# Kernel tuning notes

Measured on AMD Instinct MI355X. Metric: run time of the kernel, lower is better.

The kernel has to match this reference:

```python
import jax, jax.numpy as jnp
import numpy as np

B, IN, H = 4096, 1024, 1024


def setup_inputs() -> dict:
    key = jax.random.key(0)
    ks = jax.random.split(key, 16)
    s_in = 1.0 / np.sqrt(IN)
    s_h = 1.0 / np.sqrt(H)
    d = {
        "x_t": jax.random.normal(ks[0], (B, IN), jnp.float32),
        "h_prev": jax.random.normal(ks[1], (B, H), jnp.float32),
        "c_prev": jax.random.normal(ks[2], (B, H), jnp.float32),
    }
    # input->hidden weights (with bias), stored torch-style as (out, in)
    for i, name in enumerate(["ii", "if", "ig", "io"]):
        d[f"W_{name}"] = jax.random.uniform(ks[3 + i], (H, IN), jnp.float32, -s_in, s_in)
        d[f"b_{name}"] = jax.random.uniform(ks[7 + i], (H,), jnp.float32, -s_in, s_in)
    # hidden->hidden weights (no bias)
    for i, name in enumerate(["hi", "hf", "hg", "ho"]):
        d[f"W_{name}"] = jax.random.uniform(ks[11 + i], (H, H), jnp.float32, -s_h, s_h)
    return d


def reference(x_t, h_prev, c_prev,
              W_ii, b_ii, W_if, b_if, W_ig, b_ig, W_io, b_io,
              W_hi, W_hf, W_hg, W_ho):
    # Fuse the 8 small GEMMs into 2 concatenated GEMMs (same math).
    Wx = jnp.concatenate([W_ii, W_if, W_ig, W_io], axis=0)   # (4H, IN)
    Wh = jnp.concatenate([W_hi, W_hf, W_hg, W_ho], axis=0)   # (4H, H)
    b = jnp.concatenate([b_ii, b_if, b_ig, b_io], axis=0)    # (4H,)
    gates = x_t @ Wx.T + h_prev @ Wh.T + b                    # (B, 4H)
    zi, zf, zg, zo = jnp.split(gates, 4, axis=1)
    i_t = jax.nn.sigmoid(zi)
    f_t = jax.nn.sigmoid(zf)
    g_t = jnp.tanh(zg)
    o_t = jax.nn.sigmoid(zo)
    c_t = f_t * c_prev + i_t * g_t
    h_t = o_t * jnp.tanh(c_t)
    return (h_t, c_t, (i_t, f_t, g_t, o_t))
```

## Files before the change

### kernel.cpp

```cpp
#include <hip/hip_runtime.h>

#define B_DIM 4096
#define K_TOT 2048
#define H_DIM 1024

typedef short bf16x8 __attribute__((ext_vector_type(8)));
typedef float f32x4 __attribute__((ext_vector_type(4)));
typedef unsigned short u16x8 __attribute__((ext_vector_type(8)));

typedef __attribute__((address_space(1))) const unsigned gas_u32;
typedef __attribute__((address_space(3))) unsigned las_u32;

static __device__ __forceinline__ unsigned short f2bf(float f) {
  union { float f; unsigned u; } v; v.f = f;
  unsigned r = v.u + 0x7FFF + ((v.u >> 16) & 1);
  return (unsigned short)(r >> 16);
}

__global__ void pack_all(const float* __restrict__ x, const float* __restrict__ hp,
                         const float* __restrict__ W0, const float* __restrict__ W1,
                         const float* __restrict__ W2, const float* __restrict__ W3,
                         const float* __restrict__ W4, const float* __restrict__ W5,
                         const float* __restrict__ W6, const float* __restrict__ W7,
                         u16x8* __restrict__ A, u16x8* __restrict__ Wc) {
  const int t = blockIdx.x * blockDim.x + threadIdx.x;
  const int NA = (B_DIM * K_TOT) >> 3;
  const float* src;
  u16x8* dst;
  if (t < NA) {
    int idx = t << 3;
    int b = idx >> 11;
    int k = idx & 2047;
    src = (k < 1024) ? (x + b * 1024 + k) : (hp + b * 1024 + (k - 1024));
    dst = A + t;
  } else {
    int u = t - NA;
    int idx = u << 3;
    int n = idx >> 11;
    int k = idx & 2047;
    int gate = n >> 10;
    int j = n & 1023;
    int s = (k < 1024) ? gate : gate + 4;
    const float* base =
        (s == 0) ? W0 : (s == 1) ? W1 : (s == 2) ? W2 : (s == 3) ? W3 :
        (s == 4) ? W4 : (s == 5) ? W5 : (s == 6) ? W6 : W7;
    src = base + j * 1024 + (k & 1023);
    dst = Wc + u;
  }
  float4 lo = *(const float4*)src;
  float4 hi = *(const float4*)(src + 4);
  u16x8 v;
  v[0] = f2bf(lo.x); v[1] = f2bf(lo.y); v[2] = f2bf(lo.z); v[3] = f2bf(lo.w);
  v[4] = f2bf(hi.x); v[5] = f2bf(hi.y); v[6] = f2bf(hi.z); v[7] = f2bf(hi.w);
  *dst = v;
}

static __device__ __forceinline__ float sigm(float x) {
  return 1.0f / (1.0f + __expf(-x));
}
static __device__ __forceinline__ float tanh_fast(float x) {
  x = fminf(fmaxf(x, -15.f), 15.f);
  float t = __expf(-2.0f * x);
  return (1.0f - t) / (1.0f + t);
}

__global__ __launch_bounds__(256) void gemm_lstm(
    const unsigned short* __restrict__ A,
    const unsigned short* __restrict__ W,
    const float* __restrict__ cp,
    const float* __restrict__ bii, const float* __restrict__ bif,
    const float* __restrict__ big, const float* __restrict__ bio,
    float* __restrict__ out) {
  __shared__ unsigned short As[2][128 * 32];
  __shared__ unsigned short Bs[2][128 * 32];
  const int tid = threadIdx.x;
  const int wave = tid >> 6;
  const int lane = tid & 63;
  const int m0 = blockIdx.y << 7;
  const int j0 = blockIdx.x << 5;
  const int wm = (wave >> 1) << 6;
  const int wj16 = (wave & 1) << 4;

  f32x4 acc[4][4];
#pragma unroll
  for (int mi = 0; mi < 4; ++mi)
#pragma unroll
    for (int ni = 0; ni < 4; ++ni)
      acc[mi][ni] = (f32x4){0.f, 0.f, 0.f, 0.f};

  const int c0 = wave * 2;
  const int lr = lane >> 2;
  const int ls = lane & 3;
  const int g  = ls ^ ((lr >> 1) & 3);
  const unsigned short* aptr0 = A + (long)(m0 + c0 * 16 + lr) * K_TOT + g * 8;
  const unsigned short* aptr1 = aptr0 + 16 * K_TOT;
  const int rr0 = c0 * 16 + lr;
  const int rr1 = rr0 + 16;
  const unsigned short* bptr0 =
      W + (long)((rr0 >> 5) * 1024 + j0 + (rr0 & 31)) * K_TOT + g * 8;
  const unsigned short* bptr1 =
      W + (long)((rr1 >> 5) * 1024 + j0 + (rr1 & 31)) * K_TOT + g * 8;
  const int stg_off = c0 * 1024;

#define STAGE(buf, kk)                                                                   \
  do {                                                                                   \
    char* la = (char*)As + (buf) * 8192 + stg_off;                                       \
    char* lb = (char*)Bs + (buf) * 8192 + stg_off;                                       \
    __builtin_amdgcn_global_load_lds((gas_u32*)(aptr0 + (kk)), (las_u32*)la, 16, 0, 0);  \
    __builtin_amdgcn_global_load_lds((gas_u32*)(aptr1 + (kk)), (las_u32*)(la + 1024), 16, 0, 0); \
    __builtin_amdgcn_global_load_lds((gas_u32*)(bptr0 + (kk)), (las_u32*)lb, 16, 0, 0);  \
    __builtin_amdgcn_global_load_lds((gas_u32*)(bptr1 + (kk)), (las_u32*)(lb + 1024), 16, 0, 0); \
  } while (0)

  const int fr = lane & 15;
  const int gg = lane >> 4;
  const int sl = (gg ^ ((fr >> 1) & 3)) * 16;

  STAGE(0, 0);
  __syncthreads();

  int cur = 0;
  for (int k0 = 0; k0 < K_TOT; k0 += 32) {
    if (k0 + 32 < K_TOT) STAGE(cur ^ 1, k0 + 32);
    const char* baseA = (const char*)As + cur * 8192;
    const char* baseB = (const char*)Bs + cur * 8192;
    bf16x8 af[4], bfv[4];
#pragma unroll
    for (int i = 0; i < 4; ++i) {
      af[i]  = *(const bf16x8*)(baseA + (wm + i * 16 + fr) * 64 + sl);
      bfv[i] = *(const bf16x8*)(baseB + (i * 32 + wj16 + fr) * 64 + sl);
    }
#pragma unroll
    for (int mi = 0; mi < 4; ++mi)
#pragma unroll
      for (int ni = 0; ni < 4; ++ni)
        acc[mi][ni] = __builtin_amdgcn_mfma_f32_16x16x32_bf16(af[mi], bfv[ni], acc[mi][ni], 0, 0, 0);
    __syncthreads();
    cur ^= 1;
  }
#undef STAGE

  const int ccol = lane & 15;
  const int crow = (lane >> 4) * 4;
  const int j = j0 + wj16 + ccol;
  const float bi = bii[j];
  const float bff = bif[j];
  const float bg = big[j];
  const float bo = bio[j];
  const long BH = (long)B_DIM * H_DIM;
#pragma unroll
  for (int mi = 0; mi < 4; ++mi) {
#pragma unroll
    for (int reg = 0; reg < 4; ++reg) {
      const int row = m0 + wm + mi * 16 + crow + reg;
      const long p = (long)row * H_DIM + j;
      const float cvp = cp[p];
      const float iv = sigm(acc[mi][0][reg] + bi);
      const float fv = sigm(acc[mi][1][reg] + bff);
      const float gv = tanh_fast(acc[mi][2][reg] + bg);
      const float ov = sigm(acc[mi][3][reg] + bo);
      const float cv = fv * cvp + iv * gv;
      const float hv = ov * tanh_fast(cv);
      __builtin_nontemporal_store(hv, &out[p]);
      __builtin_nontemporal_store(cv, &out[BH + p]);
      __builtin_nontemporal_store(iv, &out[2 * BH + p]);
      __builtin_nontemporal_store(fv, &out[3 * BH + p]);
      __builtin_nontemporal_store(gv, &out[4 * BH + p]);
      __builtin_nontemporal_store(ov, &out[5 * BH + p]);
    }
  }
}

extern "C" void kernel_launch(void* const* d_in, const int* in_sizes, int n_in,
                              void* d_out, int out_size, void* d_ws, size_t ws_size,
                              hipStream_t stream) {
  const float* x    = (const float*)d_in[0];
  const float* h    = (const float*)d_in[1];
  const float* c    = (const float*)d_in[2];
  const float* W_ii = (const float*)d_in[3];
  const float* b_ii = (const float*)d_in[4];
  const float* W_if = (const float*)d_in[5];
  const float* b_if = (const float*)d_in[6];
  const float* W_ig = (const float*)d_in[7];
  const float* b_ig = (const float*)d_in[8];
  const float* W_io = (const float*)d_in[9];
  const float* b_io = (const float*)d_in[10];
  const float* W_hi = (const float*)d_in[11];
  const float* W_hf = (const float*)d_in[12];
  const float* W_hg = (const float*)d_in[13];
  const float* W_ho = (const float*)d_in[14];

  unsigned short* Abf = (unsigned short*)d_ws;
  unsigned short* Wbf = (unsigned short*)((char*)d_ws + (size_t)16 * 1024 * 1024);

  pack_all<<<8192, 256, 0, stream>>>(x, h, W_ii, W_if, W_ig, W_io,
                                     W_hi, W_hf, W_hg, W_ho,
                                     (u16x8*)Abf, (u16x8*)Wbf);
  dim3 grid(H_DIM / 32, B_DIM / 128);
  gemm_lstm<<<grid, 256, 0, stream>>>(Abf, Wbf, c, b_ii, b_if, b_ig, b_io,
                                      (float*)d_out);
}
```

Measured before the change: 287.6 us.

## Enlarge GEMM tile to 256x256 with deep multi-stage LDS pipeline

```diff
diff --git a/kernel.cpp b/kernel.cpp
--- a/kernel.cpp
+++ b/kernel.cpp
@@ -34,18 +34,21 @@
     src = (k < 1024) ? (x + b * 1024 + k) : (hp + b * 1024 + (k - 1024));
     dst = A + t;
   } else {
-    int u = t - NA;
-    int idx = u << 3;
-    int n = idx >> 11;
+    int u_ = t - NA;
+    int idx = u_ << 3;
+    int R = idx >> 11;
     int k = idx & 2047;
-    int gate = n >> 10;
-    int j = n & 1023;
+    int uu = R & 255;
+    int gate = (uu >> 4) & 3;
+    int ngg = uu >> 6;
+    int cc = uu & 15;
+    int j = (R >> 8) * 64 + ngg * 16 + cc;
     int s = (k < 1024) ? gate : gate + 4;
     const float* base =
         (s == 0) ? W0 : (s == 1) ? W1 : (s == 2) ? W2 : (s == 3) ? W3 :
         (s == 4) ? W4 : (s == 5) ? W5 : (s == 6) ? W6 : W7;
     src = base + j * 1024 + (k & 1023);
-    dst = Wc + u;
+    dst = Wc + u_;
   }
   float4 lo = *(const float4*)src;
   float4 hi = *(const float4*)(src + 4);
@@ -64,95 +67,142 @@
   return (1.0f - t) / (1.0f + t);
 }
 
-__global__ __launch_bounds__(256) void gemm_lstm(
+__global__ __launch_bounds__(512, 2) void gemm_lstm(
     const unsigned short* __restrict__ A,
     const unsigned short* __restrict__ W,
     const float* __restrict__ cp,
     const float* __restrict__ bii, const float* __restrict__ bif,
     const float* __restrict__ big, const float* __restrict__ bio,
     float* __restrict__ out) {
-  __shared__ unsigned short As[2][128 * 32];
-  __shared__ unsigned short Bs[2][128 * 32];
+  extern __shared__ char lds[];
   const int tid = threadIdx.x;
-  const int wave = tid >> 6;
+  const int w = tid >> 6;
   const int lane = tid & 63;
-  const int m0 = blockIdx.y << 7;
-  const int j0 = blockIdx.x << 5;
-  const int wm = (wave >> 1) << 6;
-  const int wj16 = (wave & 1) << 4;
-
-  f32x4 acc[4][4];
-#pragma unroll
-  for (int mi = 0; mi < 4; ++mi)
-#pragma unroll
-    for (int ni = 0; ni < 4; ++ni)
-      acc[mi][ni] = (f32x4){0.f, 0.f, 0.f, 0.f};
-
-  const int c0 = wave * 2;
-  const int lr = lane >> 2;
-  const int ls = lane & 3;
-  const int g  = ls ^ ((lr >> 1) & 3);
-  const unsigned short* aptr0 = A + (long)(m0 + c0 * 16 + lr) * K_TOT + g * 8;
-  const unsigned short* aptr1 = aptr0 + 16 * K_TOT;
-  const int rr0 = c0 * 16 + lr;
-  const int rr1 = rr0 + 16;
-  const unsigned short* bptr0 =
-      W + (long)((rr0 >> 5) * 1024 + j0 + (rr0 & 31)) * K_TOT + g * 8;
-  const unsigned short* bptr1 =
-      W + (long)((rr1 >> 5) * 1024 + j0 + (rr1 & 31)) * K_TOT + g * 8;
-  const int stg_off = c0 * 1024;
-
-#define STAGE(buf, kk)                                                                   \
-  do {                                                                                   \
-    char* la = (char*)As + (buf) * 8192 + stg_off;                                       \
-    char* lb = (char*)Bs + (buf) * 8192 + stg_off;                                       \
-    __builtin_amdgcn_global_load_lds((gas_u32*)(aptr0 + (kk)), (las_u32*)la, 16, 0, 0);  \
-    __builtin_amdgcn_global_load_lds((gas_u32*)(aptr1 + (kk)), (las_u32*)(la + 1024), 16, 0, 0); \
-    __builtin_amdgcn_global_load_lds((gas_u32*)(bptr0 + (kk)), (las_u32*)lb, 16, 0, 0);  \
-    __builtin_amdgcn_global_load_lds((gas_u32*)(bptr1 + (kk)), (las_u32*)(lb + 1024), 16, 0, 0); \
-  } while (0)
+  const int wm = w >> 2;
+  const int ng = w & 3;
+  const int bx = blockIdx.x;
+  const int by = blockIdx.y;
+
+  f32x4 acc[8][4];
+#pragma unroll
+  for (int i = 0; i < 8; ++i)
+#pragma unroll
+    for (int n = 0; n < 4; ++n)
+      acc[i][n] = (f32x4){0.f, 0.f, 0.f, 0.f};
+
+  const int v0 = tid, v1 = tid + 512;
+  const int r0 = v0 >> 2, g0 = (v0 & 3) ^ ((r0 >> 1) & 3);
+  const int r1 = v1 >> 2, g1 = (v1 & 3) ^ ((r1 >> 1) & 3);
+  const unsigned short* srcA0 = A + (long)(by * 256 + r0) * K_TOT + g0 * 8;
+  const unsigned short* srcA1 = A + (long)(by * 256 + r1) * K_TOT + g1 * 8;
+  const unsigned short* srcB0 = W + (long)(bx * 256 + r0) * K_TOT + g0 * 8;
+  const unsigned short* srcB1 = W + (long)(bx * 256 + r1) * K_TOT + g1 * 8;
+  const int d0 = v0 << 4, d1 = v1 << 4;
 
   const int fr = lane & 15;
   const int gg = lane >> 4;
-  const int sl = (gg ^ ((fr >> 1) & 3)) * 16;
-
-  STAGE(0, 0);
-  __syncthreads();
-
-  int cur = 0;
-  for (int k0 = 0; k0 < K_TOT; k0 += 32) {
-    if (k0 + 32 < K_TOT) STAGE(cur ^ 1, k0 + 32);
-    const char* baseA = (const char*)As + cur * 8192;
-    const char* baseB = (const char*)Bs + cur * 8192;
-    bf16x8 af[4], bfv[4];
-#pragma unroll
-    for (int i = 0; i < 4; ++i) {
-      af[i]  = *(const bf16x8*)(baseA + (wm + i * 16 + fr) * 64 + sl);
-      bfv[i] = *(const bf16x8*)(baseB + (i * 32 + wj16 + fr) * 64 + sl);
-    }
-#pragma unroll
-    for (int mi = 0; mi < 4; ++mi)
-#pragma unroll
-      for (int ni = 0; ni < 4; ++ni)
-        acc[mi][ni] = __builtin_amdgcn_mfma_f32_16x16x32_bf16(af[mi], bfv[ni], acc[mi][ni], 0, 0, 0);
-    __syncthreads();
-    cur ^= 1;
-  }
+  const int aoff = fr * 64 + ((gg ^ ((fr >> 1) & 3)) << 4);
+  const int wmoff = wm << 13;
+  const int ngoff = ng << 12;
+
+  bf16x8 bfr[4];
+
+#define STAGE(H)                                                               \
+  {                                                                            \
+    const int H_ = (H);                                                        \
+    const int koff_ = (H_ >> 1) * 32;                                          \
+    char* dst_ = lds + (((H_ >> 2) & 1) << 16) + ((H_ & 1) << 15) +            \
+                 (((H_ >> 1) & 1) << 14);                                      \
+    if (H_ & 1) {                                                              \
+      __builtin_amdgcn_global_load_lds((gas_u32*)(srcB0 + koff_),              \
+                                       (las_u32*)(dst_ + d0), 16, 0, 0);       \
+      __builtin_amdgcn_global_load_lds((gas_u32*)(srcB1 + koff_),              \
+                                       (las_u32*)(dst_ + d1), 16, 0, 0);       \
+    } else {                                                                   \
+      __builtin_amdgcn_global_load_lds((gas_u32*)(srcA0 + koff_),              \
+                                       (las_u32*)(dst_ + d0), 16, 0, 0);       \
+      __builtin_amdgcn_global_load_lds((gas_u32*)(srcA1 + koff_),              \
+                                       (las_u32*)(dst_ + d1), 16, 0, 0);       \
+    }                                                                          \
+  }
+
+#define G8 asm volatile("s_waitcnt vmcnt(8)" ::: "memory")
+#define G4 asm volatile("s_waitcnt vmcnt(4)" ::: "memory")
+#define G0 asm volatile("s_waitcnt vmcnt(0)" ::: "memory")
+#define GN ((void)0)
+
+#define DO_PHASE(P, KT, GUARD, DOSTAGE)                                        \
+  {                                                                            \
+    const char* lA_ = ldsbuf + ((P) >> 1) * 16384;                             \
+    const char* lB_ = ldsbuf + 32768 + ((P) >> 1) * 16384;                     \
+    bf16x8 af_[4];                                                             \
+    _Pragma("unroll")                                                          \
+    for (int i_ = 0; i_ < 4; ++i_)                                             \
+      af_[i_] = *(const bf16x8*)(lA_ + wmoff + (((P) & 1) * 4 + i_) * 1024 + aoff); \
+    if (((P) & 1) == 0) {                                                      \
+      _Pragma("unroll")                                                        \
+      for (int n_ = 0; n_ < 4; ++n_)                                           \
+        bfr[n_] = *(const bf16x8*)(lB_ + ngoff + n_ * 1024 + aoff);            \
+    }                                                                          \
+    if (DOSTAGE) STAGE((KT) * 4 + (P) + 6);                                    \
+    GUARD;                                                                     \
+    __builtin_amdgcn_s_barrier();                                              \
+    asm volatile("s_waitcnt lgkmcnt(0)" ::: "memory");                         \
+    __builtin_amdgcn_sched_barrier(0);                                         \
+    __builtin_amdgcn_s_setprio(1);                                             \
+    _Pragma("unroll")                                                          \
+    for (int i_ = 0; i_ < 4; ++i_) {                                           \
+      _Pragma("unroll")                                                        \
+      for (int n_ = 0; n_ < 4; ++n_)                                           \
+        acc[((P) & 1) * 4 + i_][n_] = __builtin_amdgcn_mfma_f32_16x16x32_bf16( \
+            af_[i_], bfr[n_], acc[((P) & 1) * 4 + i_][n_], 0, 0, 0);           \
+    }                                                                          \
+    __builtin_amdgcn_s_setprio(0);                                             \
+    __builtin_amdgcn_s_barrier();                                              \
+  }
+
+  STAGE(0); STAGE(1); STAGE(2); STAGE(3); STAGE(4); STAGE(5);
+  asm volatile("s_waitcnt vmcnt(8)" ::: "memory");
+  __builtin_amdgcn_s_barrier();
+
+  for (int kt = 0; kt < 30; ++kt) {
+    const char* ldsbuf = lds + ((kt & 1) << 16);
+    DO_PHASE(0, kt, GN, 1);
+    DO_PHASE(1, kt, G8, 1);
+    DO_PHASE(2, kt, GN, 1);
+    DO_PHASE(3, kt, G8, 1);
+  }
+  {
+    const char* ldsbuf = lds;
+    DO_PHASE(0, 30, GN, 1);
+    DO_PHASE(1, 30, G8, 1);
+    DO_PHASE(2, 30, GN, 0);
+    DO_PHASE(3, 30, G4, 0);
+  }
+  {
+    const char* ldsbuf = lds + 65536;
+    DO_PHASE(0, 31, GN, 0);
+    DO_PHASE(1, 31, G0, 0);
+    DO_PHASE(2, 31, GN, 0);
+    DO_PHASE(3, 31, GN, 0);
+  }
+#undef DO_PHASE
 #undef STAGE
 
   const int ccol = lane & 15;
-  const int crow = (lane >> 4) * 4;
-  const int j = j0 + wj16 + ccol;
+  const int crow = (lane >> 4) << 2;
+  const int j = (bx << 6) + (ng << 4) + ccol;
   const float bi = bii[j];
   const float bff = bif[j];
   const float bg = big[j];
   const float bo = bio[j];
   const long BH = (long)B_DIM * H_DIM;
-#pragma unroll
-  for (int mi = 0; mi < 4; ++mi) {
+  const int row0 = (by << 8) + (wm << 7) + crow;
+#pragma unroll
+  for (int mi = 0; mi < 8; ++mi) {
 #pragma unroll
     for (int reg = 0; reg < 4; ++reg) {
-      const int row = m0 + wm + mi * 16 + crow + reg;
+      const int row = row0 + mi * 16 + reg;
       const long p = (long)row * H_DIM + j;
       const float cvp = cp[p];
       const float iv = sigm(acc[mi][0][reg] + bi);
@@ -161,12 +211,12 @@
       const float ov = sigm(acc[mi][3][reg] + bo);
       const float cv = fv * cvp + iv * gv;
       const float hv = ov * tanh_fast(cv);
-      __builtin_nontemporal_store(hv, &out[p]);
-      __builtin_nontemporal_store(cv, &out[BH + p]);
-      __builtin_nontemporal_store(iv, &out[2 * BH + p]);
-      __builtin_nontemporal_store(fv, &out[3 * BH + p]);
-      __builtin_nontemporal_store(gv, &out[4 * BH + p]);
-      __builtin_nontemporal_store(ov, &out[5 * BH + p]);
+      out[p]          = hv;
+      out[BH + p]     = cv;
+      out[2 * BH + p] = iv;
+      out[3 * BH + p] = fv;
+      out[4 * BH + p] = gv;
+      out[5 * BH + p] = ov;
     }
   }
 }
@@ -193,10 +243,17 @@
   unsigned short* Abf = (unsigned short*)d_ws;
   unsigned short* Wbf = (unsigned short*)((char*)d_ws + (size_t)16 * 1024 * 1024);
 
+  static bool s_attr = false;
+  if (!s_attr) {
+    hipFuncSetAttribute((const void*)gemm_lstm,
+                        hipFuncAttributeMaxDynamicSharedMemorySize, 131072);
+    s_attr = true;
+  }
+
   pack_all<<<8192, 256, 0, stream>>>(x, h, W_ii, W_if, W_ig, W_io,
                                      W_hi, W_hf, W_hg, W_ho,
                                      (u16x8*)Abf, (u16x8*)Wbf);
-  dim3 grid(H_DIM / 32, B_DIM / 128);
-  gemm_lstm<<<grid, 256, 0, stream>>>(Abf, Wbf, c, b_ii, b_if, b_ig, b_io,
-                                      (float*)d_out);
-}
+  dim3 grid(H_DIM / 64, B_DIM / 256);
+  gemm_lstm<<<grid, 512, 131072, stream>>>(Abf, Wbf, c, b_ii, b_if, b_ig, b_io,
+                                           (float*)d_out);
+}
```

New measurement: 259.6 us. 1.11x faster.
